# Kernel tuning notes

Hardware: AMD Instinct MI355X
Metric: run time of the kernel (lower is better)

The kernel has to match this reference:

```python
import jax, jax.numpy as jnp
import numpy as np

D_MODEL = 1024
NHEAD = 16
HEAD_DIM = D_MODEL // NHEAD


def setup_inputs() -> dict:
    key = jax.random.key(0)
    ks = jax.random.split(key, 7)
    N, S, E = 2, 2048, D_MODEL
    query = jax.random.normal(ks[0], (N, S, E), dtype=jnp.float32)
    key_t = jax.random.normal(ks[1], (N, S, E), dtype=jnp.float32)
    value = jax.random.normal(ks[2], (N, S, E), dtype=jnp.float32)
    # nn.Linear default init scale ~ 1/sqrt(fan_in)
    s = 1.0 / np.sqrt(E)
    w_in = jax.random.uniform(ks[3], (3 * E, E), jnp.float32, -s, s)
    b_in = jax.random.uniform(ks[4], (3 * E,), jnp.float32, -s, s)
    w_o = jax.random.uniform(ks[5], (E, E), jnp.float32, -s, s)
    b_o = jax.random.uniform(ks[6], (E,), jnp.float32, -s, s)
    return {"query": query, "key": key_t, "value": value,
            "w_in": w_in, "b_in": b_in, "w_o": w_o, "b_o": b_o}


def reference(query, key, value, w_in, b_in, w_o, b_o):
    # NOTE: the torch module computes q,k,v all from `query` (self-attention);
    # the `key`/`value` args are ignored by its forward math.
    N, S, E = query.shape
    H, Dh = NHEAD, HEAD_DIM
    qkv = query @ w_in.T + b_in                      # (N, S, 3E)
    q, k, v = jnp.split(qkv, 3, axis=-1)
    def heads(x):
        return x.reshape(N, S, H, Dh).transpose(0, 2, 1, 3)  # (N, H, S, Dh)
    q, k, v = heads(q), heads(k), heads(v)
    scale = 1.0 / jnp.sqrt(jnp.asarray(Dh, query.dtype))
    scores = jnp.einsum('bhqd,bhkd->bhqk', q, k) * scale     # (N, H, S, S)
    attn = jax.nn.softmax(scores, axis=-1)
    out = jnp.einsum('bhqk,bhkd->bhqd', attn, v)             # (N, H, S, Dh)
    out = out.transpose(0, 2, 1, 3).reshape(N, S, E)
    return out @ w_o.T + b_o
```

## Files before the change

kernel.cpp:

```cpp
#include <hip/hip_runtime.h>
#include <hip/hip_bf16.h>
#include <stdint.h>

#define NB   2
#define SEQ  2048
#define EMB  1024
#define NH   16
#define DH   64
#define MR   (NB*SEQ)
#define E3   (3*EMB)
#define CSC  (0.125f * 1.44269504f)

typedef __attribute__((ext_vector_type(8))) short bf16x8;
typedef __attribute__((ext_vector_type(4))) float f32x4;
typedef __attribute__((ext_vector_type(16))) float f32x16;

__device__ __forceinline__ unsigned short f2bf(float f) {
  unsigned u = __float_as_uint(f);
  unsigned r = (u + 0x7FFF + ((u >> 16) & 1)) >> 16;
  return (unsigned short)r;
}
__device__ __forceinline__ unsigned pack2(float lo, float hi) {
  return (unsigned)f2bf(lo) | ((unsigned)f2bf(hi) << 16);
}
__device__ __forceinline__ float bf2f(unsigned short s) {
  return __uint_as_float(((unsigned)s) << 16);
}
__device__ __forceinline__ unsigned cvtpk(float lo, float hi) {
  unsigned r;
  asm("v_cvt_pk_bf16_f32 %0, %1, %2" : "=v"(r) : "v"(lo), "v"(hi));
  return r;
}

__device__ __forceinline__ void gld16(const unsigned short* g, unsigned short* l) {
  __builtin_amdgcn_global_load_lds(
      (const __attribute__((address_space(1))) unsigned int*)g,
      (__attribute__((address_space(3))) unsigned int*)l,
      16, 0, 0);
}

__global__ void cvt_all(const float* __restrict__ q,
                        const float* __restrict__ w_in,
                        const float* __restrict__ w_o,
                        unsigned short* __restrict__ Xbf,
                        unsigned short* __restrict__ Winbf,
                        unsigned short* __restrict__ Wobf) {
  int b = blockIdx.x;
  const float* src; unsigned short* dst; int off;
  if (b < 2048)      { src = q;    dst = Xbf;   off = b; }
  else if (b < 3584) { src = w_in; dst = Winbf; off = b - 2048; }
  else               { src = w_o;  dst = Wobf;  off = b - 3584; }
  int i = (off * 256 + threadIdx.x) * 8;
  float4 a = *(const float4*)(src + i);
  float4 c = *(const float4*)(src + i + 4);
  uint4 o;
  o.x = pack2(a.x, a.y);
  o.y = pack2(a.z, a.w);
  o.z = pack2(c.x, c.y);
  o.w = pack2(c.z, c.w);
  *(uint4*)(dst + i) = o;
}

template<int BN, bool OUT_F32>
__global__ __launch_bounds__(256) void gemm_bt(
    const unsigned short* __restrict__ A,
    const unsigned short* __restrict__ Bt,
    const float* __restrict__ bias,
    void* __restrict__ Cout,
    int K, int ldc, int scale_cols) {
  constexpr int NR = BN / 32;
  constexpr int WNT = BN / 2;
  __shared__ unsigned short As[4096];
  __shared__ unsigned short Bs[BN * 32];
  const int tid  = threadIdx.x;
  const int lane = tid & 63;
  const int w    = tid >> 6;
  const int wm = w >> 1, wn = w & 1;
  const int g = lane >> 4, li = lane & 15;
  const int rowBase = blockIdx.x * 128;
  const int colBase = blockIdx.y * BN;

  f32x4 acc[4][NR];
#pragma unroll
  for (int m = 0; m < 4; ++m)
#pragma unroll
    for (int nn = 0; nn < NR; ++nn) { acc[m][nn][0]=0.f; acc[m][nn][1]=0.f; acc[m][nn][2]=0.f; acc[m][nn][3]=0.f; }

  const unsigned short* Ag = A  + (size_t)(rowBase + (tid >> 2)) * K + (tid & 3) * 8;
  const unsigned short* Bg = Bt + (size_t)(colBase + (tid >> 2)) * K + (tid & 3) * 8;

  for (int k0 = 0; k0 < K; k0 += 32) {
    __syncthreads();
    gld16(Ag + k0,                As + tid * 8);
    gld16(Ag + (size_t)64*K + k0, As + 2048 + tid * 8);
    gld16(Bg + k0,                Bs + tid * 8);
    if (BN == 128)
      gld16(Bg + (size_t)64*K + k0, Bs + 2048 + tid * 8);
    __syncthreads();

    bf16x8 af[4], bfv[NR];
#pragma unroll
    for (int m = 0; m < 4; ++m)
      af[m] = *(const bf16x8*)&As[(wm*64 + m*16 + li) * 32 + g * 8];
#pragma unroll
    for (int nn = 0; nn < NR; ++nn)
      bfv[nn] = *(const bf16x8*)&Bs[(wn*WNT + nn*16 + li) * 32 + g * 8];
#pragma unroll
    for (int m = 0; m < 4; ++m)
#pragma unroll
      for (int nn = 0; nn < NR; ++nn)
        acc[m][nn] = __builtin_amdgcn_mfma_f32_16x16x32_bf16(af[m], bfv[nn], acc[m][nn], 0, 0, 0);
  }

#pragma unroll
  for (int nn = 0; nn < NR; ++nn) {
    const int col = colBase + wn*WNT + nn*16 + li;
    const float bv = bias[col];
    const float sc = (col < scale_cols) ? CSC : 1.0f;
#pragma unroll
    for (int m = 0; m < 4; ++m) {
      const int r0 = rowBase + wm*64 + m*16 + g*4;
#pragma unroll
      for (int r = 0; r < 4; ++r) {
        float v = (acc[m][nn][r] + bv) * sc;
        if (OUT_F32) ((float*)Cout)[(size_t)(r0 + r) * ldc + col] = v;
        else ((unsigned short*)Cout)[(size_t)(r0 + r) * ldc + col] = f2bf(v);
      }
    }
  }
}

__global__ __launch_bounds__(256, 3) void attn32(
    const unsigned short* __restrict__ qkv,
    unsigned short* __restrict__ O0,
    unsigned short* __restrict__ O1,
    float* __restrict__ ML) {
  __shared__ unsigned short smem[16384];
  char* LB = (char*)smem;

  const int tid  = threadIdx.x;
  const int lane = tid & 63;
  const int w    = tid >> 6;
  const int hi   = lane >> 5;
  const int l31  = lane & 31;
  const int bid  = blockIdx.x;
  const int qb = bid & 15, h = (bid >> 4) & 15, n = (bid >> 8) & 1, z = bid >> 9;
  const size_t rowN = (size_t)n * SEQ;
  const int kt0 = z * 1024;
  const int vp_ = tid & 31, dblk = tid >> 5;
  const int vps = (vp_ & ~6) | ((vp_ & 2) << 1) | ((vp_ & 4) >> 1);
  unsigned short* Oz = z ? O1 : O0;

  bf16x8 qf[4];
  {
    const size_t qr = rowN + qb*128 + w*32 + l31;
#pragma unroll
    for (int kc = 0; kc < 4; ++kc)
      qf[kc] = *(const bf16x8*)&qkv[qr * E3 + h*64 + kc*16 + hi*8];
  }

  f32x16 ZEROV;
#pragma unroll
  for (int i = 0; i < 16; ++i) ZEROV[i] = 0.f;
  f32x16 acc0 = ZEROV, acc1 = ZEROV;
  float ssum[8];
#pragma unroll
  for (int i = 0; i < 8; ++i) ssum[i] = 0.f;

  uint4 pv0, pv1;
  auto stageK = [&](int kt, int buf) {
#pragma unroll
    for (int p = 0; p < 2; ++p) {
      int r = p*32 + (tid >> 3);
      int ch = (tid & 7) ^ (r & 7);
      gld16(&qkv[(rowN + kt + r) * E3 + EMB + h*64 + ch*8],
            &smem[buf*4096 + p*2048 + tid*8]);
    }
  };
  auto loadV = [&](int kt) {
    const unsigned short* vp = &qkv[(rowN + kt + 2*vp_) * E3 + 2*EMB + h*64 + dblk*8];
    pv0 = *(const uint4*)vp;
    pv1 = *(const uint4*)(vp + E3);
  };
  auto writeV = [&](int buf) {
    const unsigned short* s0 = (const unsigned short*)&pv0;
    const unsigned short* s1 = (const unsigned short*)&pv1;
#pragma unroll
    for (int j = 0; j < 8; ++j) {
      int d = dblk*8 + j;
      unsigned val = (unsigned)s0[j] | ((unsigned)s1[j] << 16);
      *(unsigned*)(LB + 16384 + buf*8192 + d*128 + (((vps>>2) ^ (d&7)) << 4) + (vps&3)*4) = val;
    }
  };

  loadV(kt0);
  stageK(kt0, 0);
  writeV(0);
  __syncthreads();

  for (int t = 0; t < 16; ++t) {
    const int cur = t & 1;
    const bool pre = (t + 1 < 16);
    const int ktn = kt0 + (t + 1) * 64;
    if (pre) { loadV(ktn); stageK(ktn, cur^1); }

    const char* Kb = LB + cur*8192;
    bf16x8 ka[4], kb[4];
#pragma unroll
    for (int kc = 0; kc < 4; ++kc) {
      const int sw = ((kc*2 + hi) ^ (l31 & 7)) << 4;
      ka[kc] = *(const bf16x8*)(Kb + l31*128 + sw);
      kb[kc] = *(const bf16x8*)(Kb + 4096 + l31*128 + sw);
    }
    __builtin_amdgcn_s_setprio(1);
    f32x16 z0 = __builtin_amdgcn_mfma_f32_32x32x16_bf16(ka[0], qf[0], ZEROV, 0, 0, 0);
    f32x16 z1 = __builtin_amdgcn_mfma_f32_32x32x16_bf16(kb[0], qf[0], ZEROV, 0, 0, 0);
#pragma unroll
    for (int kc = 1; kc < 4; ++kc) {
      z0 = __builtin_amdgcn_mfma_f32_32x32x16_bf16(ka[kc], qf[kc], z0, 0, 0, 0);
      z1 = __builtin_amdgcn_mfma_f32_32x32x16_bf16(kb[kc], qf[kc], z1, 0, 0, 0);
    }
    __builtin_amdgcn_s_setprio(0);

#pragma unroll
    for (int i = 0; i < 16; ++i) {
      z0[i] = __builtin_amdgcn_exp2f(z0[i]);
      z1[i] = __builtin_amdgcn_exp2f(z1[i]);
    }
#pragma unroll
    for (int i = 0; i < 8; ++i)
      ssum[i] += (z0[2*i] + z0[2*i+1]) + (z1[2*i] + z1[2*i+1]);

    bf16x8 pf[4];
    {
      union { bf16x8 v; unsigned u[4]; } r0_, r1_, r2_, r3_;
#pragma unroll
      for (int j = 0; j < 4; ++j) {
        r0_.u[j] = cvtpk(z0[2*j],     z0[2*j + 1]);
        r1_.u[j] = cvtpk(z0[8 + 2*j], z0[9 + 2*j]);
        r2_.u[j] = cvtpk(z1[2*j],     z1[2*j + 1]);
        r3_.u[j] = cvtpk(z1[8 + 2*j], z1[9 + 2*j]);
      }
      pf[0] = r0_.v; pf[1] = r1_.v; pf[2] = r2_.v; pf[3] = r3_.v;
    }

    if (pre) writeV(cur ^ 1);

    const char* Vb = LB + 16384 + cur*8192;
    __builtin_amdgcn_s_setprio(1);
#pragma unroll
    for (int c = 0; c < 4; ++c) {
      const int sw = ((c*2 + hi) ^ (l31 & 7)) << 4;
      bf16x8 va = *(const bf16x8*)(Vb + l31*128 + sw);
      bf16x8 vb = *(const bf16x8*)(Vb + 4096 + l31*128 + sw);
      acc0 = __builtin_amdgcn_mfma_f32_32x32x16_bf16(va, pf[c], acc0, 0, 0, 0);
      acc1 = __builtin_amdgcn_mfma_f32_32x32x16_bf16(vb, pf[c], acc1, 0, 0, 0);
    }
    __builtin_amdgcn_s_setprio(0);
    __syncthreads();
  }

#pragma unroll
  for (int st = 4; st; st >>= 1)
#pragma unroll
    for (int i = 0; i < st; ++i) ssum[i] += ssum[i + st];
  float lsum = ssum[0] + __shfl_xor(ssum[0], 32);

  const int qrow_l = w*32 + l31;
  if (hi == 0) {
    size_t grow = rowN + qb*128 + qrow_l;
    ML[(size_t)z*65536 + grow*16 + h] = lsum;
  }

  float rn = 1.0f / lsum;
#pragma unroll
  for (int dt = 0; dt < 2; ++dt) {
#pragma unroll
    for (int r = 0; r < 16; r += 2) {
      float v0 = (dt ? acc1[r]   : acc0[r])   * rn;
      float v1 = (dt ? acc1[r+1] : acc0[r+1]) * rn;
      int d = dt*32 + (r & 3) + 8*(r >> 2) + 4*hi;
      unsigned val = pack2(v0, v1);
      int col32 = d >> 1;
      int g = col32 >> 2;
      *(unsigned*)(LB + qrow_l*128 + ((g ^ (qrow_l & 7)) << 4) + (col32 & 3)*4) = val;
    }
  }
  __syncthreads();
  {
    int row = tid >> 1;
    size_t orow = (rowN + qb*128 + row) * EMB + h*64;
#pragma unroll
    for (int i = 0; i < 4; ++i) {
      int gg = (tid & 1)*4 + i;
      uint4 v = *(const uint4*)(LB + row*128 + ((gg ^ (row & 7)) << 4));
      *(uint4*)&Oz[orow + gg*8] = v;
    }
  }
}

__global__ void attn_combine(const unsigned short* __restrict__ O0,
                             const unsigned short* __restrict__ O1,
                             const float* __restrict__ ML,
                             unsigned short* __restrict__ x2) {
  int idx = (blockIdx.x * 256 + threadIdx.x) * 8;
  int row = idx >> 10;
  int h = (idx & 1023) >> 6;
  float l0 = ML[row*16 + h];
  float l1 = ML[65536 + row*16 + h];
  float rl = 1.0f / (l0 + l1);
  float w0 = l0 * rl, w1 = l1 * rl;
  uint4 u0 = *(const uint4*)(O0 + idx);
  uint4 u1 = *(const uint4*)(O1 + idx);
  const unsigned* p0 = (const unsigned*)&u0;
  const unsigned* p1 = (const unsigned*)&u1;
  uint4 o;
  unsigned* po = (unsigned*)&o;
#pragma unroll
  for (int j = 0; j < 4; ++j) {
    float lo = w0 * bf2f((unsigned short)(p0[j] & 0xFFFF))
             + w1 * bf2f((unsigned short)(p1[j] & 0xFFFF));
    float hv = w0 * bf2f((unsigned short)(p0[j] >> 16))
             + w1 * bf2f((unsigned short)(p1[j] >> 16));
    po[j] = pack2(lo, hv);
  }
  *(uint4*)(x2 + idx) = o;
}

extern "C" void kernel_launch(void* const* d_in, const int* in_sizes, int n_in,
                              void* d_out, int out_size, void* d_ws, size_t ws_size,
                              hipStream_t stream) {
  const float* q    = (const float*)d_in[0];
  const float* w_in = (const float*)d_in[3];
  const float* b_in = (const float*)d_in[4];
  const float* w_o  = (const float*)d_in[5];
  const float* b_o  = (const float*)d_in[6];

  char* ws = (char*)d_ws;
  unsigned short* Wobf  = (unsigned short*)(ws);
  unsigned short* Xbf   = (unsigned short*)(ws + 2097152);
  unsigned short* Winbf = (unsigned short*)(ws + 10485760);
  unsigned short* QKV   = (unsigned short*)(ws + 16777216);
  unsigned short* X2    = (unsigned short*)(ws + 41943040);
  unsigned short* O0    = Xbf;
  unsigned short* O1    = X2;
  float*          ML    = (float*)(ws + 10485760);

  cvt_all<<<4096, 256, 0, stream>>>(q, w_in, w_o, Xbf, Winbf, Wobf);

  gemm_bt<128, false><<<dim3(32, 24), 256, 0, stream>>>(Xbf, Winbf, b_in, (void*)QKV, EMB, E3, 1024);
  attn32<<<NB * NH * (SEQ / 128) * 2, 256, 0, stream>>>(QKV, O0, O1, ML);
  attn_combine<<<2048, 256, 0, stream>>>(O0, O1, ML, X2);
  gemm_bt<64, true><<<dim3(32, 16), 256, 0, stream>>>(X2, Wobf, b_o, d_out, EMB, EMB, 0);
}
```

Baseline: 125.7 us.

## Fuse split-K attention combine into output projection GEMM and remap attention blocks

Removes the separate attn_combine kernel. The output-projection GEMM now loads both partial attention outputs plus their softmax sums, merges them in registers and writes the merged A-tile straight into shared memory. This saves one launch and a full write and read of the intermediate X2 buffer. In exchange, each of the 16 column blocks redoes the combine for the same rows, the A loads become synchronous register loads instead of direct-to-LDS loads, and each tile needs extra ML loads and a division. Attention block indices are also permuted so that the z halves and neighbouring heads are interleaved differently across the launch order, which may change cache locality.

```diff
diff --git a/kernel.cpp b/kernel.cpp
--- a/kernel.cpp
+++ b/kernel.cpp
@@ -61,30 +61,27 @@
   *(uint4*)(dst + i) = o;
 }
 
-template<int BN, bool OUT_F32>
 __global__ __launch_bounds__(256) void gemm_bt(
     const unsigned short* __restrict__ A,
     const unsigned short* __restrict__ Bt,
     const float* __restrict__ bias,
-    void* __restrict__ Cout,
+    unsigned short* __restrict__ Cout,
     int K, int ldc, int scale_cols) {
-  constexpr int NR = BN / 32;
-  constexpr int WNT = BN / 2;
   __shared__ unsigned short As[4096];
-  __shared__ unsigned short Bs[BN * 32];
+  __shared__ unsigned short Bs[4096];
   const int tid  = threadIdx.x;
   const int lane = tid & 63;
   const int w    = tid >> 6;
   const int wm = w >> 1, wn = w & 1;
   const int g = lane >> 4, li = lane & 15;
   const int rowBase = blockIdx.x * 128;
-  const int colBase = blockIdx.y * BN;
-
-  f32x4 acc[4][NR];
+  const int colBase = blockIdx.y * 128;
+
+  f32x4 acc[4][4];
 #pragma unroll
   for (int m = 0; m < 4; ++m)
 #pragma unroll
-    for (int nn = 0; nn < NR; ++nn) { acc[m][nn][0]=0.f; acc[m][nn][1]=0.f; acc[m][nn][2]=0.f; acc[m][nn][3]=0.f; }
+    for (int nn = 0; nn < 4; ++nn) { acc[m][nn][0]=0.f; acc[m][nn][1]=0.f; acc[m][nn][2]=0.f; acc[m][nn][3]=0.f; }
 
   const unsigned short* Ag = A  + (size_t)(rowBase + (tid >> 2)) * K + (tid & 3) * 8;
   const unsigned short* Bg = Bt + (size_t)(colBase + (tid >> 2)) * K + (tid & 3) * 8;
@@ -94,27 +91,26 @@
     gld16(Ag + k0,                As + tid * 8);
     gld16(Ag + (size_t)64*K + k0, As + 2048 + tid * 8);
     gld16(Bg + k0,                Bs + tid * 8);
-    if (BN == 128)
-      gld16(Bg + (size_t)64*K + k0, Bs + 2048 + tid * 8);
+    gld16(Bg + (size_t)64*K + k0, Bs + 2048 + tid * 8);
     __syncthreads();
 
-    bf16x8 af[4], bfv[NR];
+    bf16x8 af[4], bfv[4];
 #pragma unroll
     for (int m = 0; m < 4; ++m)
       af[m] = *(const bf16x8*)&As[(wm*64 + m*16 + li) * 32 + g * 8];
 #pragma unroll
-    for (int nn = 0; nn < NR; ++nn)
-      bfv[nn] = *(const bf16x8*)&Bs[(wn*WNT + nn*16 + li) * 32 + g * 8];
+    for (int nn = 0; nn < 4; ++nn)
+      bfv[nn] = *(const bf16x8*)&Bs[(wn*64 + nn*16 + li) * 32 + g * 8];
 #pragma unroll
     for (int m = 0; m < 4; ++m)
 #pragma unroll
-      for (int nn = 0; nn < NR; ++nn)
+      for (int nn = 0; nn < 4; ++nn)
         acc[m][nn] = __builtin_amdgcn_mfma_f32_16x16x32_bf16(af[m], bfv[nn], acc[m][nn], 0, 0, 0);
   }
 
 #pragma unroll
-  for (int nn = 0; nn < NR; ++nn) {
-    const int col = colBase + wn*WNT + nn*16 + li;
+  for (int nn = 0; nn < 4; ++nn) {
+    const int col = colBase + wn*64 + nn*16 + li;
     const float bv = bias[col];
     const float sc = (col < scale_cols) ? CSC : 1.0f;
 #pragma unroll
@@ -123,9 +119,92 @@
 #pragma unroll
       for (int r = 0; r < 4; ++r) {
         float v = (acc[m][nn][r] + bv) * sc;
-        if (OUT_F32) ((float*)Cout)[(size_t)(r0 + r) * ldc + col] = v;
-        else ((unsigned short*)Cout)[(size_t)(r0 + r) * ldc + col] = f2bf(v);
+        Cout[(size_t)(r0 + r) * ldc + col] = f2bf(v);
       }
+    }
+  }
+}
+
+__global__ __launch_bounds__(256) void gemm_out(
+    const unsigned short* __restrict__ O0,
+    const unsigned short* __restrict__ O1,
+    const float* __restrict__ ML,
+    const unsigned short* __restrict__ Bt,
+    const float* __restrict__ bias,
+    float* __restrict__ Cout) {
+  __shared__ unsigned short As[4096];
+  __shared__ unsigned short Bs[2048];
+  const int tid  = threadIdx.x;
+  const int lane = tid & 63;
+  const int w    = tid >> 6;
+  const int wm = w >> 1, wn = w & 1;
+  const int g = lane >> 4, li = lane & 15;
+  const int rowBase = blockIdx.x * 128;
+  const int colBase = blockIdx.y * 64;
+
+  f32x4 acc[4][2];
+#pragma unroll
+  for (int m = 0; m < 4; ++m)
+#pragma unroll
+    for (int nn = 0; nn < 2; ++nn) { acc[m][nn][0]=0.f; acc[m][nn][1]=0.f; acc[m][nn][2]=0.f; acc[m][nn][3]=0.f; }
+
+  const int arow = tid >> 2;
+  const int acol = (tid & 3) * 8;
+  const unsigned short* Bg = Bt + (size_t)(colBase + (tid >> 2)) * EMB + (tid & 3) * 8;
+
+  for (int k0 = 0; k0 < 1024; k0 += 32) {
+    const int h = k0 >> 6;
+    __syncthreads();
+    gld16(Bg + k0, Bs + tid * 8);
+#pragma unroll
+    for (int p = 0; p < 2; ++p) {
+      const int r = rowBase + p*64 + arow;
+      float l0 = ML[r*16 + h];
+      float l1 = ML[65536 + r*16 + h];
+      float rl = 1.0f / (l0 + l1);
+      float w0 = l0 * rl, w1 = l1 * rl;
+      uint4 u0 = *(const uint4*)&O0[(size_t)r * EMB + k0 + acol];
+      uint4 u1 = *(const uint4*)&O1[(size_t)r * EMB + k0 + acol];
+      const unsigned* p0 = (const unsigned*)&u0;
+      const unsigned* p1 = (const unsigned*)&u1;
+      uint4 o;
+      unsigned* po = (unsigned*)&o;
+#pragma unroll
+      for (int j = 0; j < 4; ++j) {
+        float lo = w0 * bf2f((unsigned short)(p0[j] & 0xFFFF))
+                 + w1 * bf2f((unsigned short)(p1[j] & 0xFFFF));
+        float hv = w0 * bf2f((unsigned short)(p0[j] >> 16))
+                 + w1 * bf2f((unsigned short)(p1[j] >> 16));
+        po[j] = pack2(lo, hv);
+      }
+      *(uint4*)&As[p*2048 + tid*8] = o;
+    }
+    __syncthreads();
+
+    bf16x8 af[4], bfv[2];
+#pragma unroll
+    for (int m = 0; m < 4; ++m)
+      af[m] = *(const bf16x8*)&As[(wm*64 + m*16 + li) * 32 + g * 8];
+#pragma unroll
+    for (int nn = 0; nn < 2; ++nn)
+      bfv[nn] = *(const bf16x8*)&Bs[(wn*32 + nn*16 + li) * 32 + g * 8];
+#pragma unroll
+    for (int m = 0; m < 4; ++m)
+#pragma unroll
+      for (int nn = 0; nn < 2; ++nn)
+        acc[m][nn] = __builtin_amdgcn_mfma_f32_16x16x32_bf16(af[m], bfv[nn], acc[m][nn], 0, 0, 0);
+  }
+
+#pragma unroll
+  for (int nn = 0; nn < 2; ++nn) {
+    const int col = colBase + wn*32 + nn*16 + li;
+    const float bv = bias[col];
+#pragma unroll
+    for (int m = 0; m < 4; ++m) {
+      const int r0 = rowBase + wm*64 + m*16 + g*4;
+#pragma unroll
+      for (int r = 0; r < 4; ++r)
+        Cout[(size_t)(r0 + r) * EMB + col] = acc[m][nn][r] + bv;
     }
   }
 }
@@ -143,7 +222,8 @@
   const int w    = tid >> 6;
   const int hi   = lane >> 5;
   const int l31  = lane & 31;
-  const int bid  = blockIdx.x;
+  const int slot = blockIdx.x;
+  const int bid  = (slot & 7) * 128 + (slot >> 3);
   const int qb = bid & 15, h = (bid >> 4) & 15, n = (bid >> 8) & 1, z = bid >> 9;
   const size_t rowN = (size_t)n * SEQ;
   const int kt0 = z * 1024;
@@ -299,34 +379,6 @@
   }
 }
 
-__global__ void attn_combine(const unsigned short* __restrict__ O0,
-                             const unsigned short* __restrict__ O1,
-                             const float* __restrict__ ML,
-                             unsigned short* __restrict__ x2) {
-  int idx = (blockIdx.x * 256 + threadIdx.x) * 8;
-  int row = idx >> 10;
-  int h = (idx & 1023) >> 6;
-  float l0 = ML[row*16 + h];
-  float l1 = ML[65536 + row*16 + h];
-  float rl = 1.0f / (l0 + l1);
-  float w0 = l0 * rl, w1 = l1 * rl;
-  uint4 u0 = *(const uint4*)(O0 + idx);
-  uint4 u1 = *(const uint4*)(O1 + idx);
-  const unsigned* p0 = (const unsigned*)&u0;
-  const unsigned* p1 = (const unsigned*)&u1;
-  uint4 o;
-  unsigned* po = (unsigned*)&o;
-#pragma unroll
-  for (int j = 0; j < 4; ++j) {
-    float lo = w0 * bf2f((unsigned short)(p0[j] & 0xFFFF))
-             + w1 * bf2f((unsigned short)(p1[j] & 0xFFFF));
-    float hv = w0 * bf2f((unsigned short)(p0[j] >> 16))
-             + w1 * bf2f((unsigned short)(p1[j] >> 16));
-    po[j] = pack2(lo, hv);
-  }
-  *(uint4*)(x2 + idx) = o;
-}
-
 extern "C" void kernel_launch(void* const* d_in, const int* in_sizes, int n_in,
                               void* d_out, int out_size, void* d_ws, size_t ws_size,
                               hipStream_t stream) {
@@ -348,8 +400,7 @@
 
   cvt_all<<<4096, 256, 0, stream>>>(q, w_in, w_o, Xbf, Winbf, Wobf);
 
-  gemm_bt<128, false><<<dim3(32, 24), 256, 0, stream>>>(Xbf, Winbf, b_in, (void*)QKV, EMB, E3, 1024);
+  gemm_bt<<<dim3(32, 24), 256, 0, stream>>>(Xbf, Winbf, b_in, QKV, EMB, E3, 1024);
   attn32<<<NB * NH * (SEQ / 128) * 2, 256, 0, stream>>>(QKV, O0, O1, ML);
-  attn_combine<<<2048, 256, 0, stream>>>(O0, O1, ML, X2);
-  gemm_bt<64, true><<<dim3(32, 16), 256, 0, stream>>>(X2, Wobf, b_o, d_out, EMB, EMB, 0);
-}
+  gemm_out<<<dim3(32, 16), 256, 0, stream>>>(O0, O1, ML, Wobf, b_o, (float*)d_out);
+}
```

Result: slower. 143.3 us (+14.0%).
